# Performance work log

Measured on AMD Instinct MI355X. Metric: run time of the kernel, lower is better.

Reference implementation:

```python
import jax, jax.numpy as jnp
import numpy as np


def _silu(v):
    return v * jax.nn.sigmoid(v)


def setup_inputs() -> dict:
    key = jax.random.key(0)
    ks = jax.random.split(key, 12)
    B, N, DS = 4, 12500, 63      # batch, nodes per graph, dim_single
    E = 800000                   # total edges (avg degree 16)
    BN = B * N
    ND = DS + 1                  # node_dim = dim_single + 1 (timestep channel)
    H, ED = 128, 32              # hidden_dim, edge_dim (fixed in __init__)
    MIN = 2 * ND + ED            # m_input feature dim = 160

    def lin(k, i, o):
        return (jax.random.normal(k, (i, o)) / np.sqrt(i)).astype(jnp.float32)

    return {
        "x": jax.random.normal(ks[0], (B, N, 3), dtype=jnp.float32) * 5.0,
        "cond": jax.random.normal(ks[1], (B, N, DS), dtype=jnp.float32),
        "edge_dist": jax.random.uniform(ks[2], (E,), dtype=jnp.float32) * 15.0,
        "ew1": lin(ks[3], 1, ED), "eb1": jnp.zeros((ED,), jnp.float32),
        "ew2": lin(ks[4], ED, ED), "eb2": jnp.zeros((ED,), jnp.float32),
        "nw1": lin(ks[5], MIN, H), "nb1": jnp.zeros((H,), jnp.float32),
        "nw2": lin(ks[6], H, ND), "nb2": jnp.zeros((ND,), jnp.float32),
        "cw1": lin(ks[7], MIN, H), "cb1": jnp.zeros((H,), jnp.float32),
        "cw2": lin(ks[8], H, 1),
        "edge_index": jax.random.randint(ks[9], (2, E), 0, BN, dtype=jnp.int64 if jax.config.jax_enable_x64 else jnp.int32),
        "t": 100,
    }


def reference(x, cond, edge_dist, ew1, eb1, ew2, eb2, nw1, nb1, nw2, nb2,
              cw1, cb1, cw2, edge_index, t):
    B, N, _ = x.shape
    BN = B * N
    # append timestep scalar channel to conditioning -> node features h
    t_feat = jnp.full((B, N, 1), t, dtype=x.dtype)
    h = jnp.concatenate([cond, t_feat], axis=-1).reshape(BN, -1)   # [BN, node_dim]
    xf = x.reshape(BN, 3)

    src, dst = edge_index[0], edge_index[1]
    # edge_mlp on scalar distances -> [E, edge_dim]
    edge_attr = _silu(edge_dist[:, None] @ ew1 + eb1) @ ew2 + eb2
    # gather + concat -> [E, 2*node_dim + edge_dim]
    m_input = jnp.concatenate([h[src], h[dst], edge_attr], axis=-1)
    # node_mlp (its output h_agg is discarded by p_sample, kept for faithfulness)
    m = _silu(m_input @ nw1 + nb1) @ nw2 + nb2
    h_agg = jax.ops.segment_sum(m, dst, num_segments=BN)
    h_out = h + h_agg  # unused by p_sample's return
    del h_out
    # coord_mlp -> scalar weight per edge
    coord_weight = _silu(m_input @ cw1 + cb1) @ cw2                 # [E, 1]
    dir_vec = xf[src] - xf[dst]                                     # [E, 3]
    dir_len = jnp.maximum(jnp.linalg.norm(dir_vec, axis=-1, keepdims=True), 1e-8)
    coord_update = coord_weight * (dir_vec / dir_len)
    x_agg = jax.ops.segment_sum(coord_update, dst, num_segments=BN)
    return (xf + x_agg).reshape(B, N, 3)
```

## Files before the change

### kernel.cpp

```cpp
#include <hip/hip_runtime.h>
#include <hip/hip_bf16.h>

typedef __attribute__((ext_vector_type(8))) short bf16x8;
typedef __attribute__((ext_vector_type(4))) float f32x4;
typedef __attribute__((ext_vector_type(4), aligned(4))) float f32x4u;
typedef __attribute__((ext_vector_type(2), aligned(4))) float f32x2u;

__device__ __forceinline__ unsigned short f2bf(float f) {
    unsigned int u = __float_as_uint(f);
    unsigned int r = (u + 0x7fffu + ((u >> 16) & 1u)) >> 16;
    return (unsigned short)r;
}
__device__ __forceinline__ float bflo(unsigned int u) { return __uint_as_float(u << 16); }
__device__ __forceinline__ float bfhi(unsigned int u) { return __uint_as_float(u & 0xffff0000u); }

__global__ void prep_merged_kernel(
    const float* __restrict__ x, float* __restrict__ out, int n_out,
    const float* __restrict__ cw1, unsigned short* __restrict__ bt2,
    const float* __restrict__ ew2, const float* __restrict__ eb2,
    const float* __restrict__ cb1, const int* __restrict__ tptr,
    unsigned short* __restrict__ bt_M, float* __restrict__ c0)
{
    const int b = blockIdx.x, tid = threadIdx.x;
    if (b < 64) {
        int idx = b * 256 + tid;
        int n = idx >> 6, k = idx & 63;
        float v = 0.f;
        if (k < 63) v = (n < 128) ? cw1[k * 128 + n] : cw1[(64 + k) * 128 + (n - 128)];
        bt2[n * 64 + k] = f2bf(v);
    } else if (b == 64) {
        if (tid < 128) {
            int j = tid;
            float t = (float)tptr[0];
            float cacc = cb1[j] + t * (cw1[63 * 128 + j] + cw1[127 * 128 + j]);
            float m[32];
            #pragma unroll
            for (int p = 0; p < 32; ++p) m[p] = 0.f;
            for (int i = 0; i < 32; ++i) {
                float w = cw1[(128 + i) * 128 + j];
                cacc = fmaf(eb2[i], w, cacc);
                #pragma unroll
                for (int p = 0; p < 32; ++p) m[p] = fmaf(ew2[p * 32 + i], w, m[p]);
            }
            c0[j] = cacc;
            #pragma unroll
            for (int p = 0; p < 32; ++p) bt_M[j * 32 + p] = f2bf(m[p]);
        }
    } else {
        int i = (b - 65) * 256 + tid;
        if (i < n_out) out[i] = x[i];
    }
}

__device__ __forceinline__ bf16x8 load8_bf(const float* p) {
    f32x4u a = *(const f32x4u*)p;
    f32x4u b = *(const f32x4u*)(p + 4);
    bf16x8 r;
    r[0] = f2bf(a[0]); r[1] = f2bf(a[1]); r[2] = f2bf(a[2]); r[3] = f2bf(a[3]);
    r[4] = f2bf(b[0]); r[5] = f2bf(b[1]); r[6] = f2bf(b[2]); r[7] = f2bf(b[3]);
    return r;
}
__device__ __forceinline__ bf16x8 load7z_bf(const float* p) {
    f32x4u a = *(const f32x4u*)p;
    f32x2u b = *(const f32x2u*)(p + 4);
    float c = p[6];
    bf16x8 r;
    r[0] = f2bf(a[0]); r[1] = f2bf(a[1]); r[2] = f2bf(a[2]); r[3] = f2bf(a[3]);
    r[4] = f2bf(b[0]); r[5] = f2bf(b[1]); r[6] = f2bf(c);  r[7] = 0;
    return r;
}

__global__ __launch_bounds__(256) void prep_uv_kernel(
    const float* __restrict__ cond, const unsigned short* __restrict__ bt2,
    unsigned short* __restrict__ UV, int BN)
{
    const int tid = threadIdx.x, lane = tid & 63, wid = tid >> 6;
    const int fr = lane & 15, kq = lane >> 4;
    int node = blockIdx.x * 64 + wid * 16 + fr;
    if (node >= BN) node = BN - 1;

    const float* cp = cond + (long)node * 63;
    bf16x8 b0 = load8_bf(cp + 8 * kq);
    bf16x8 b1 = (kq < 3) ? load8_bf(cp + 32 + 8 * kq) : load7z_bf(cp + 56);

    char* UVb = (char*)UV;
    const unsigned nb = (unsigned)node * 512u + (unsigned)(kq * 64);

    #pragma unroll
    for (int n = 0; n < 16; ++n) {
        bf16x8 a0 = *reinterpret_cast<const bf16x8*>(&bt2[(n * 16 + fr) * 64 + 8 * kq]);
        bf16x8 a1 = *reinterpret_cast<const bf16x8*>(&bt2[(n * 16 + fr) * 64 + 32 + 8 * kq]);
        f32x4 acc = (f32x4){0.f, 0.f, 0.f, 0.f};
        acc = __builtin_amdgcn_mfma_f32_16x16x32_bf16(a0, b0, acc, 0, 0, 0);
        acc = __builtin_amdgcn_mfma_f32_16x16x32_bf16(a1, b1, acc, 0, 0, 0);
        uint2 pk;
        pk.x = (unsigned)f2bf(acc[0]) | ((unsigned)f2bf(acc[1]) << 16);
        pk.y = (unsigned)f2bf(acc[2]) | ((unsigned)f2bf(acc[3]) << 16);
        unsigned off = nb + ((n & 8) ? 256u : 0u) + (unsigned)((n & 7) * 8);
        *reinterpret_cast<uint2*>(UVb + off) = pk;
    }
}

__global__ __launch_bounds__(256, 3) void edge_kernel(
    const float* __restrict__ x, const float* __restrict__ edge_dist,
    const float* __restrict__ ew1, const float* __restrict__ eb1,
    const unsigned short* __restrict__ bt_M, const float* __restrict__ c0f,
    const float* __restrict__ cw2, const unsigned short* __restrict__ UV,
    const int* __restrict__ edge_index, float* __restrict__ out, int E)
{
    __shared__ __align__(16) unsigned short s_lds[128][40];
    __shared__ int srcl[128];
    __shared__ int dstl[128];
    __shared__ float cw_lds[128];

    const int tid = threadIdx.x, lane = tid & 63, wid = tid >> 6;
    const int fr = lane & 15, kq = lane >> 4;
    const int e0 = blockIdx.x * 128;

    if (tid < 128) {
        int e = e0 + tid; if (e >= E) e = E - 1;
        float dist = edge_dist[e];
        #pragma unroll
        for (int i = 0; i < 16; ++i) {
            float v0 = fmaf(dist, ew1[2 * i],     eb1[2 * i]);
            float v1 = fmaf(dist, ew1[2 * i + 1], eb1[2 * i + 1]);
            float s0 = v0 / (1.f + __expf(-v0));
            float s1 = v1 / (1.f + __expf(-v1));
            unsigned pk = (unsigned)f2bf(s0) | ((unsigned)f2bf(s1) << 16);
            *reinterpret_cast<unsigned*>(&s_lds[tid][2 * i]) = pk;
        }
    } else {
        int r = tid - 128;
        int e = e0 + r; if (e >= E) e = E - 1;
        srcl[r] = edge_index[e];
        dstl[r] = edge_index[E + e];
    }
    __syncthreads();

    bf16x8 sb[2];
    #pragma unroll
    for (int m = 0; m < 2; ++m)
        sb[m] = *reinterpret_cast<const bf16x8*>(&s_lds[wid * 32 + m * 16 + fr][8 * kq]);

    unsigned bu[2], bv[2];
    #pragma unroll
    for (int m = 0; m < 2; ++m) {
        int row = wid * 32 + m * 16 + fr;
        bu[m] = (unsigned)srcl[row] * 512u + (unsigned)(kq * 64);
        bv[m] = (unsigned)dstl[row] * 512u + 256u + (unsigned)(kq * 64);
    }

    const char* UVb = (const char*)UV;
    uint4 Lu[2][4], Lv[2][4];
    #pragma unroll
    for (int m = 0; m < 2; ++m)
        #pragma unroll
        for (int i = 0; i < 4; ++i) {
            Lu[m][i] = *reinterpret_cast<const uint4*>(UVb + bu[m] + i * 16);
            Lv[m][i] = *reinterpret_cast<const uint4*>(UVb + bv[m] + i * 16);
        }

    float psum[2] = {0.f, 0.f};
    #pragma unroll
    for (int nh = 0; nh < 2; ++nh) {
        f32x4 acc[2][4];
        #pragma unroll
        for (int n = 0; n < 4; ++n) {
            f32x4u c = *reinterpret_cast<const f32x4u*>(c0f + (nh * 4 + n) * 16 + kq * 4);
            acc[0][n] = (f32x4){c[0], c[1], c[2], c[3]};
            acc[1][n] = acc[0][n];
        }
        #pragma unroll
        for (int n = 0; n < 4; ++n) {
            bf16x8 aw = *reinterpret_cast<const bf16x8*>(&bt_M[((nh * 4 + n) * 16 + fr) * 32 + 8 * kq]);
            acc[0][n] = __builtin_amdgcn_mfma_f32_16x16x32_bf16(aw, sb[0], acc[0][n], 0, 0, 0);
            acc[1][n] = __builtin_amdgcn_mfma_f32_16x16x32_bf16(aw, sb[1], acc[1][n], 0, 0, 0);
        }
        #pragma unroll
        for (int n = 0; n < 4; ++n) {
            const int g = nh * 4 + n;
            f32x4u w2 = *reinterpret_cast<const f32x4u*>(cw2 + g * 16 + kq * 4);
            #pragma unroll
            for (int m = 0; m < 2; ++m) {
                unsigned du0 = (g & 1) ? Lu[m][g >> 1].z : Lu[m][g >> 1].x;
                unsigned du1 = (g & 1) ? Lu[m][g >> 1].w : Lu[m][g >> 1].y;
                unsigned dv0 = (g & 1) ? Lv[m][g >> 1].z : Lv[m][g >> 1].x;
                unsigned dv1 = (g & 1) ? Lv[m][g >> 1].w : Lv[m][g >> 1].y;
                float uf[4] = {bflo(du0), bfhi(du0), bflo(du1), bfhi(du1)};
                float vf[4] = {bflo(dv0), bfhi(dv0), bflo(dv1), bfhi(dv1)};
                #pragma unroll
                for (int r = 0; r < 4; ++r) {
                    float h = acc[m][n][r] + uf[r] + vf[r];
                    float sil = h / (1.f + __expf(-h));
                    psum[m] = fmaf(sil, w2[r], psum[m]);
                }
            }
        }
    }

    #pragma unroll
    for (int m = 0; m < 2; ++m) {
        psum[m] += __shfl_xor(psum[m], 16, 64);
        psum[m] += __shfl_xor(psum[m], 32, 64);
    }
    if (kq == 0) {
        #pragma unroll
        for (int m = 0; m < 2; ++m)
            cw_lds[wid * 32 + m * 16 + fr] = psum[m];
    }
    __syncthreads();

    if (tid < 128) {
        int e = e0 + tid;
        if (e < E) {
            float coord_w = cw_lds[tid];
            int src = srcl[tid];
            int dst = dstl[tid];
            float dx = x[src * 3 + 0] - x[dst * 3 + 0];
            float dy = x[src * 3 + 1] - x[dst * 3 + 1];
            float dz = x[src * 3 + 2] - x[dst * 3 + 2];
            float len = sqrtf(fmaf(dx, dx, fmaf(dy, dy, dz * dz)));
            len = fmaxf(len, 1e-8f);
            float sc = coord_w / len;
            atomicAdd(&out[dst * 3 + 0], sc * dx);
            atomicAdd(&out[dst * 3 + 1], sc * dy);
            atomicAdd(&out[dst * 3 + 2], sc * dz);
        }
    }
}

extern "C" void kernel_launch(void* const* d_in, const int* in_sizes, int n_in,
                              void* d_out, int out_size, void* d_ws, size_t ws_size,
                              hipStream_t stream) {
    const float* x         = (const float*)d_in[0];
    const float* cond      = (const float*)d_in[1];
    const float* edge_dist = (const float*)d_in[2];
    const float* ew1       = (const float*)d_in[3];
    const float* eb1       = (const float*)d_in[4];
    const float* ew2       = (const float*)d_in[5];
    const float* eb2       = (const float*)d_in[6];
    const float* cw1       = (const float*)d_in[11];
    const float* cb1       = (const float*)d_in[12];
    const float* cw2       = (const float*)d_in[13];
    const int*   edge_index= (const int*)d_in[14];
    const int*   tptr      = (const int*)d_in[15];
    float* out = (float*)d_out;

    const int E  = in_sizes[2];
    const int BN = in_sizes[1] / 63;
    const int n_out = out_size;

    char* ws = (char*)d_ws;
    unsigned short* bt_M = (unsigned short*)(ws);
    float*          c0   = (float*)(ws + 8192);
    unsigned short* bt2  = (unsigned short*)(ws + 16384);
    unsigned short* UV   = (unsigned short*)(ws + 65536);

    int init_blocks = (n_out + 255) / 256;
    prep_merged_kernel<<<65 + init_blocks, 256, 0, stream>>>(
        x, out, n_out, cw1, bt2, ew2, eb2, cb1, tptr, bt_M, c0);
    prep_uv_kernel<<<(BN + 63) / 64, 256, 0, stream>>>(cond, bt2, UV, BN);

    int blocks = (E + 127) / 128;
    edge_kernel<<<blocks, 256, 0, stream>>>(x, edge_dist, ew1, eb1,
                                            bt_M, c0, cw2, UV,
                                            edge_index, out, E);
}
```

Before: 303.5 us.

## Merge prep kernels, make edge kernel wave-local without block barriers

Folds the weight transpose and the per-node UV projection into one prep kernel. Each block rebuilds the bf16 weight tile in padded LDS, which removes one launch and the global bt2 round trip. The edge kernel now has each wave load its own indices and compute its own edge-MLP rows, and it replaces __syncthreads with s_waitcnt so waves run independently. The UV layout is interleaved so that U+V can be folded into the MFMA accumulator init. Occupancy hint rises to 4 blocks. The risk is that LDS visibility within a wave depends on the inline waitcnt, and every prep block redundantly converts cw1.

Result: faster. 271.5 us (-10.5%).

```diff
diff --git a/kernel.cpp b/kernel.cpp
--- a/kernel.cpp
+++ b/kernel.cpp
@@ -14,21 +14,67 @@
 __device__ __forceinline__ float bflo(unsigned int u) { return __uint_as_float(u << 16); }
 __device__ __forceinline__ float bfhi(unsigned int u) { return __uint_as_float(u & 0xffff0000u); }
 
-__global__ void prep_merged_kernel(
+__device__ __forceinline__ bf16x8 load8_bf(const float* p) {
+    f32x4u a = *(const f32x4u*)p;
+    f32x4u b = *(const f32x4u*)(p + 4);
+    bf16x8 r;
+    r[0] = f2bf(a[0]); r[1] = f2bf(a[1]); r[2] = f2bf(a[2]); r[3] = f2bf(a[3]);
+    r[4] = f2bf(b[0]); r[5] = f2bf(b[1]); r[6] = f2bf(b[2]); r[7] = f2bf(b[3]);
+    return r;
+}
+__device__ __forceinline__ bf16x8 load7z_bf(const float* p) {
+    f32x4u a = *(const f32x4u*)p;
+    f32x2u b = *(const f32x2u*)(p + 4);
+    float c = p[6];
+    bf16x8 r;
+    r[0] = f2bf(a[0]); r[1] = f2bf(a[1]); r[2] = f2bf(a[2]); r[3] = f2bf(a[3]);
+    r[4] = f2bf(b[0]); r[5] = f2bf(b[1]); r[6] = f2bf(c);  r[7] = 0;
+    return r;
+}
+
+__global__ __launch_bounds__(256) void prep_kernel(
     const float* __restrict__ x, float* __restrict__ out, int n_out,
-    const float* __restrict__ cw1, unsigned short* __restrict__ bt2,
+    const float* __restrict__ cond, const float* __restrict__ cw1,
     const float* __restrict__ ew2, const float* __restrict__ eb2,
     const float* __restrict__ cb1, const int* __restrict__ tptr,
-    unsigned short* __restrict__ bt_M, float* __restrict__ c0)
+    unsigned short* __restrict__ bt_M, float* __restrict__ c0,
+    unsigned short* __restrict__ UV, int BN, int nb_uv)
 {
     const int b = blockIdx.x, tid = threadIdx.x;
-    if (b < 64) {
-        int idx = b * 256 + tid;
-        int n = idx >> 6, k = idx & 63;
-        float v = 0.f;
-        if (k < 63) v = (n < 128) ? cw1[k * 128 + n] : cw1[(64 + k) * 128 + (n - 128)];
-        bt2[n * 64 + k] = f2bf(v);
-    } else if (b == 64) {
+    if (b < nb_uv) {
+        __shared__ __align__(16) unsigned short bt2[256 * 72];
+        {
+            const int c = tid;
+            const float* colp = (c < 128) ? (cw1 + c) : (cw1 + 64 * 128 + (c - 128));
+            for (int k = 0; k < 63; ++k)
+                bt2[c * 72 + k] = f2bf(colp[k * 128]);
+            bt2[c * 72 + 63] = 0;
+        }
+        __syncthreads();
+
+        const int lane = tid & 63, wid = tid >> 6;
+        const int fr = lane & 15, kq = lane >> 4;
+        int node = b * 64 + wid * 16 + fr;
+        if (node >= BN) node = BN - 1;
+        const float* cp = cond + (long)node * 63;
+        bf16x8 b0 = load8_bf(cp + 8 * kq);
+        bf16x8 b1 = (kq < 3) ? load8_bf(cp + 32 + 8 * kq) : load7z_bf(cp + 56);
+
+        char* UVb = (char*)UV;
+        const unsigned off0 = (unsigned)node * 512u + (unsigned)(kq * 8);
+        #pragma unroll
+        for (int n = 0; n < 16; ++n) {
+            bf16x8 a0 = *reinterpret_cast<const bf16x8*>(&bt2[(n * 16 + fr) * 72 + 8 * kq]);
+            bf16x8 a1 = *reinterpret_cast<const bf16x8*>(&bt2[(n * 16 + fr) * 72 + 32 + 8 * kq]);
+            f32x4 acc = (f32x4){0.f, 0.f, 0.f, 0.f};
+            acc = __builtin_amdgcn_mfma_f32_16x16x32_bf16(a0, b0, acc, 0, 0, 0);
+            acc = __builtin_amdgcn_mfma_f32_16x16x32_bf16(a1, b1, acc, 0, 0, 0);
+            uint2 pk;
+            pk.x = (unsigned)f2bf(acc[0]) | ((unsigned)f2bf(acc[1]) << 16);
+            pk.y = (unsigned)f2bf(acc[2]) | ((unsigned)f2bf(acc[3]) << 16);
+            *reinterpret_cast<uint2*>(UVb + off0 + n * 32) = pk;
+        }
+    } else if (b == nb_uv) {
         if (tid < 128) {
             int j = tid;
             float t = (float)tptr[0];
@@ -47,61 +93,12 @@
             for (int p = 0; p < 32; ++p) bt_M[j * 32 + p] = f2bf(m[p]);
         }
     } else {
-        int i = (b - 65) * 256 + tid;
+        int i = (b - nb_uv - 1) * 256 + tid;
         if (i < n_out) out[i] = x[i];
     }
 }
 
-__device__ __forceinline__ bf16x8 load8_bf(const float* p) {
-    f32x4u a = *(const f32x4u*)p;
-    f32x4u b = *(const f32x4u*)(p + 4);
-    bf16x8 r;
-    r[0] = f2bf(a[0]); r[1] = f2bf(a[1]); r[2] = f2bf(a[2]); r[3] = f2bf(a[3]);
-    r[4] = f2bf(b[0]); r[5] = f2bf(b[1]); r[6] = f2bf(b[2]); r[7] = f2bf(b[3]);
-    return r;
-}
-__device__ __forceinline__ bf16x8 load7z_bf(const float* p) {
-    f32x4u a = *(const f32x4u*)p;
-    f32x2u b = *(const f32x2u*)(p + 4);
-    float c = p[6];
-    bf16x8 r;
-    r[0] = f2bf(a[0]); r[1] = f2bf(a[1]); r[2] = f2bf(a[2]); r[3] = f2bf(a[3]);
-    r[4] = f2bf(b[0]); r[5] = f2bf(b[1]); r[6] = f2bf(c);  r[7] = 0;
-    return r;
-}
-
-__global__ __launch_bounds__(256) void prep_uv_kernel(
-    const float* __restrict__ cond, const unsigned short* __restrict__ bt2,
-    unsigned short* __restrict__ UV, int BN)
-{
-    const int tid = threadIdx.x, lane = tid & 63, wid = tid >> 6;
-    const int fr = lane & 15, kq = lane >> 4;
-    int node = blockIdx.x * 64 + wid * 16 + fr;
-    if (node >= BN) node = BN - 1;
-
-    const float* cp = cond + (long)node * 63;
-    bf16x8 b0 = load8_bf(cp + 8 * kq);
-    bf16x8 b1 = (kq < 3) ? load8_bf(cp + 32 + 8 * kq) : load7z_bf(cp + 56);
-
-    char* UVb = (char*)UV;
-    const unsigned nb = (unsigned)node * 512u + (unsigned)(kq * 64);
-
-    #pragma unroll
-    for (int n = 0; n < 16; ++n) {
-        bf16x8 a0 = *reinterpret_cast<const bf16x8*>(&bt2[(n * 16 + fr) * 64 + 8 * kq]);
-        bf16x8 a1 = *reinterpret_cast<const bf16x8*>(&bt2[(n * 16 + fr) * 64 + 32 + 8 * kq]);
-        f32x4 acc = (f32x4){0.f, 0.f, 0.f, 0.f};
-        acc = __builtin_amdgcn_mfma_f32_16x16x32_bf16(a0, b0, acc, 0, 0, 0);
-        acc = __builtin_amdgcn_mfma_f32_16x16x32_bf16(a1, b1, acc, 0, 0, 0);
-        uint2 pk;
-        pk.x = (unsigned)f2bf(acc[0]) | ((unsigned)f2bf(acc[1]) << 16);
-        pk.y = (unsigned)f2bf(acc[2]) | ((unsigned)f2bf(acc[3]) << 16);
-        unsigned off = nb + ((n & 8) ? 256u : 0u) + (unsigned)((n & 7) * 8);
-        *reinterpret_cast<uint2*>(UVb + off) = pk;
-    }
-}
-
-__global__ __launch_bounds__(256, 3) void edge_kernel(
+__global__ __launch_bounds__(256, 4) void edge_kernel(
     const float* __restrict__ x, const float* __restrict__ edge_dist,
     const float* __restrict__ ew1, const float* __restrict__ eb1,
     const unsigned short* __restrict__ bt_M, const float* __restrict__ c0f,
@@ -109,70 +106,92 @@
     const int* __restrict__ edge_index, float* __restrict__ out, int E)
 {
     __shared__ __align__(16) unsigned short s_lds[128][40];
-    __shared__ int srcl[128];
-    __shared__ int dstl[128];
+    __shared__ int idx_lds[2][128];
     __shared__ float cw_lds[128];
 
     const int tid = threadIdx.x, lane = tid & 63, wid = tid >> 6;
     const int fr = lane & 15, kq = lane >> 4;
-    const int e0 = blockIdx.x * 128;
-
-    if (tid < 128) {
-        int e = e0 + tid; if (e >= E) e = E - 1;
+    const int lp = lane & 31, hf = lane >> 5;
+    const int e0w = blockIdx.x * 128 + wid * 32;
+
+    {
+        int e = e0w + lp; if (e >= E) e = E - 1;
+        idx_lds[hf][wid * 32 + lp] = edge_index[hf ? (E + e) : e];
+    }
+    asm volatile("s_waitcnt lgkmcnt(0)" ::: "memory");
+    int srow[2], drow[2];
+    #pragma unroll
+    for (int m = 0; m < 2; ++m) {
+        srow[m] = idx_lds[0][wid * 32 + m * 16 + fr];
+        drow[m] = idx_lds[1][wid * 32 + m * 16 + fr];
+    }
+
+    const char* UVb = (const char*)UV;
+    uint2 Lu[2][8], Lv[2][8];
+    #pragma unroll
+    for (int m = 0; m < 2; ++m) {
+        unsigned bu = (unsigned)srow[m] * 512u + (unsigned)(kq * 8);
+        unsigned bv = (unsigned)drow[m] * 512u + 256u + (unsigned)(kq * 8);
+        #pragma unroll
+        for (int g = 0; g < 8; ++g) {
+            Lu[m][g] = *reinterpret_cast<const uint2*>(UVb + bu + g * 32);
+            Lv[m][g] = *reinterpret_cast<const uint2*>(UVb + bv + g * 32);
+        }
+    }
+
+    {
+        int eh = lane >> 1, j0 = (lane & 1) * 16;
+        int e = e0w + eh; if (e >= E) e = E - 1;
         float dist = edge_dist[e];
-        #pragma unroll
-        for (int i = 0; i < 16; ++i) {
-            float v0 = fmaf(dist, ew1[2 * i],     eb1[2 * i]);
-            float v1 = fmaf(dist, ew1[2 * i + 1], eb1[2 * i + 1]);
-            float s0 = v0 / (1.f + __expf(-v0));
-            float s1 = v1 / (1.f + __expf(-v1));
-            unsigned pk = (unsigned)f2bf(s0) | ((unsigned)f2bf(s1) << 16);
-            *reinterpret_cast<unsigned*>(&s_lds[tid][2 * i]) = pk;
-        }
-    } else {
-        int r = tid - 128;
-        int e = e0 + r; if (e >= E) e = E - 1;
-        srcl[r] = edge_index[e];
-        dstl[r] = edge_index[E + e];
-    }
-    __syncthreads();
+        f32x4u wv[4], bb[4];
+        #pragma unroll
+        for (int i = 0; i < 4; ++i) {
+            wv[i] = *reinterpret_cast<const f32x4u*>(ew1 + j0 + 4 * i);
+            bb[i] = *reinterpret_cast<const f32x4u*>(eb1 + j0 + 4 * i);
+        }
+        unsigned pk[8];
+        #pragma unroll
+        for (int i = 0; i < 8; ++i) {
+            float a0 = fmaf(dist, wv[i >> 1][(i & 1) * 2 + 0], bb[i >> 1][(i & 1) * 2 + 0]);
+            float a1 = fmaf(dist, wv[i >> 1][(i & 1) * 2 + 1], bb[i >> 1][(i & 1) * 2 + 1]);
+            float s0 = a0 / (1.f + __expf(-a0));
+            float s1 = a1 / (1.f + __expf(-a1));
+            pk[i] = (unsigned)f2bf(s0) | ((unsigned)f2bf(s1) << 16);
+        }
+        uint4 q0 = make_uint4(pk[0], pk[1], pk[2], pk[3]);
+        uint4 q1 = make_uint4(pk[4], pk[5], pk[6], pk[7]);
+        *reinterpret_cast<uint4*>(&s_lds[wid * 32 + eh][j0]) = q0;
+        *reinterpret_cast<uint4*>(&s_lds[wid * 32 + eh][j0 + 8]) = q1;
+    }
+    asm volatile("s_waitcnt lgkmcnt(0)" ::: "memory");
 
     bf16x8 sb[2];
     #pragma unroll
     for (int m = 0; m < 2; ++m)
         sb[m] = *reinterpret_cast<const bf16x8*>(&s_lds[wid * 32 + m * 16 + fr][8 * kq]);
 
-    unsigned bu[2], bv[2];
-    #pragma unroll
-    for (int m = 0; m < 2; ++m) {
-        int row = wid * 32 + m * 16 + fr;
-        bu[m] = (unsigned)srcl[row] * 512u + (unsigned)(kq * 64);
-        bv[m] = (unsigned)dstl[row] * 512u + 256u + (unsigned)(kq * 64);
-    }
-
-    const char* UVb = (const char*)UV;
-    uint4 Lu[2][4], Lv[2][4];
-    #pragma unroll
-    for (int m = 0; m < 2; ++m)
-        #pragma unroll
-        for (int i = 0; i < 4; ++i) {
-            Lu[m][i] = *reinterpret_cast<const uint4*>(UVb + bu[m] + i * 16);
-            Lv[m][i] = *reinterpret_cast<const uint4*>(UVb + bv[m] + i * 16);
-        }
-
     float psum[2] = {0.f, 0.f};
     #pragma unroll
     for (int nh = 0; nh < 2; ++nh) {
         f32x4 acc[2][4];
         #pragma unroll
         for (int n = 0; n < 4; ++n) {
-            f32x4u c = *reinterpret_cast<const f32x4u*>(c0f + (nh * 4 + n) * 16 + kq * 4);
-            acc[0][n] = (f32x4){c[0], c[1], c[2], c[3]};
-            acc[1][n] = acc[0][n];
+            const int g = nh * 4 + n;
+            f32x4u c = *reinterpret_cast<const f32x4u*>(c0f + g * 16 + kq * 4);
+            #pragma unroll
+            for (int m = 0; m < 2; ++m) {
+                unsigned u0 = Lu[m][g].x, u1 = Lu[m][g].y;
+                unsigned v0 = Lv[m][g].x, v1 = Lv[m][g].y;
+                acc[m][n] = (f32x4){ c[0] + bflo(u0) + bflo(v0),
+                                     c[1] + bfhi(u0) + bfhi(v0),
+                                     c[2] + bflo(u1) + bflo(v1),
+                                     c[3] + bfhi(u1) + bfhi(v1) };
+            }
         }
         #pragma unroll
         for (int n = 0; n < 4; ++n) {
-            bf16x8 aw = *reinterpret_cast<const bf16x8*>(&bt_M[((nh * 4 + n) * 16 + fr) * 32 + 8 * kq]);
+            const int g = nh * 4 + n;
+            bf16x8 aw = *reinterpret_cast<const bf16x8*>(&bt_M[(g * 16 + fr) * 32 + 8 * kq]);
             acc[0][n] = __builtin_amdgcn_mfma_f32_16x16x32_bf16(aw, sb[0], acc[0][n], 0, 0, 0);
             acc[1][n] = __builtin_amdgcn_mfma_f32_16x16x32_bf16(aw, sb[1], acc[1][n], 0, 0, 0);
         }
@@ -181,20 +200,13 @@
             const int g = nh * 4 + n;
             f32x4u w2 = *reinterpret_cast<const f32x4u*>(cw2 + g * 16 + kq * 4);
             #pragma unroll
-            for (int m = 0; m < 2; ++m) {
-                unsigned du0 = (g & 1) ? Lu[m][g >> 1].z : Lu[m][g >> 1].x;
-                unsigned du1 = (g & 1) ? Lu[m][g >> 1].w : Lu[m][g >> 1].y;
-                unsigned dv0 = (g & 1) ? Lv[m][g >> 1].z : Lv[m][g >> 1].x;
-                unsigned dv1 = (g & 1) ? Lv[m][g >> 1].w : Lv[m][g >> 1].y;
-                float uf[4] = {bflo(du0), bfhi(du0), bflo(du1), bfhi(du1)};
-                float vf[4] = {bflo(dv0), bfhi(dv0), bflo(dv1), bfhi(dv1)};
+            for (int m = 0; m < 2; ++m)
                 #pragma unroll
                 for (int r = 0; r < 4; ++r) {
-                    float h = acc[m][n][r] + uf[r] + vf[r];
+                    float h = acc[m][n][r];
                     float sil = h / (1.f + __expf(-h));
                     psum[m] = fmaf(sil, w2[r], psum[m]);
                 }
-            }
         }
     }
 
@@ -208,14 +220,13 @@
         for (int m = 0; m < 2; ++m)
             cw_lds[wid * 32 + m * 16 + fr] = psum[m];
     }
-    __syncthreads();
-
-    if (tid < 128) {
-        int e = e0 + tid;
+    asm volatile("s_waitcnt lgkmcnt(0)" ::: "memory");
+    if (lane < 32) {
+        int e = e0w + lp;
         if (e < E) {
-            float coord_w = cw_lds[tid];
-            int src = srcl[tid];
-            int dst = dstl[tid];
+            float coord_w = cw_lds[wid * 32 + lp];
+            int src = idx_lds[0][wid * 32 + lp];
+            int dst = idx_lds[1][wid * 32 + lp];
             float dx = x[src * 3 + 0] - x[dst * 3 + 0];
             float dy = x[src * 3 + 1] - x[dst * 3 + 1];
             float dz = x[src * 3 + 2] - x[dst * 3 + 2];
@@ -253,13 +264,12 @@
     char* ws = (char*)d_ws;
     unsigned short* bt_M = (unsigned short*)(ws);
     float*          c0   = (float*)(ws + 8192);
-    unsigned short* bt2  = (unsigned short*)(ws + 16384);
     unsigned short* UV   = (unsigned short*)(ws + 65536);
 
-    int init_blocks = (n_out + 255) / 256;
-    prep_merged_kernel<<<65 + init_blocks, 256, 0, stream>>>(
-        x, out, n_out, cw1, bt2, ew2, eb2, cb1, tptr, bt_M, c0);
-    prep_uv_kernel<<<(BN + 63) / 64, 256, 0, stream>>>(cond, bt2, UV, BN);
+    const int nb_uv = (BN + 63) / 64;
+    const int nb_out = (n_out + 255) / 256;
+    prep_kernel<<<nb_uv + 1 + nb_out, 256, 0, stream>>>(
+        x, out, n_out, cond, cw1, ew2, eb2, cb1, tptr, bt_M, c0, UV, BN, nb_uv);
 
     int blocks = (E + 127) / 128;
     edge_kernel<<<blocks, 256, 0, stream>>>(x, edge_dist, ew1, eb1,
```
